# Kernel tuning notes

Measured on AMD Instinct MI355X. Metric: run time of the kernel, lower is better.

Reference implementation:

```python
import jax, jax.numpy as jnp
import numpy as np

BN_EPS = 1e-5

def _conv1x1(x, w, b):
    # x: (B,C,H,W), w: (O,C), b: (O,)
    return jnp.einsum('bchw,oc->bohw', x, w) + b[None, :, None, None]

def setup_inputs() -> dict:
    key = jax.random.key(0)
    ks = jax.random.split(key, 9)
    B, C, H, W = 16, 512, 64, 64
    Ci = C // 2
    x = jax.random.normal(ks[0], (B, C, H, W), dtype=jnp.float32)
    s_in = (2.0 / C) ** 0.5   # kaiming fan_out-ish scale for 1x1 conv
    s_ci = (2.0 / Ci) ** 0.5
    return {
        'x': x,
        'g_w': jax.random.normal(ks[1], (Ci, C), dtype=jnp.float32) * s_in,
        'g_b': jnp.zeros((Ci,), dtype=jnp.float32),
        'theta_w': jax.random.normal(ks[2], (Ci, C), dtype=jnp.float32) * s_in,
        'theta_b': jnp.zeros((Ci,), dtype=jnp.float32),
        'phi_w': jax.random.normal(ks[3], (Ci, C), dtype=jnp.float32) * s_in,
        'phi_b': jnp.zeros((Ci,), dtype=jnp.float32),
        'W_w': jax.random.normal(ks[4], (C, Ci), dtype=jnp.float32) * s_ci,
        'W_b': jnp.zeros((C,), dtype=jnp.float32),
        'bn_gamma': jnp.ones((C,), dtype=jnp.float32),
        'bn_beta': jnp.zeros((C,), dtype=jnp.float32),
    }

def reference(x, g_w, g_b, theta_w, theta_b, phi_w, phi_b, W_w, W_b, bn_gamma, bn_beta):
    B, C, H, W = x.shape
    N = H * W
    g_x = _conv1x1(x, g_w, g_b).reshape(B, -1, N)          # (B, Ci, N)
    theta_x = _conv1x1(x, theta_w, theta_b).reshape(B, -1, N)  # (B, Ci, N)
    phi_x = _conv1x1(x, phi_w, phi_b).reshape(B, -1, N)        # (B, Ci, N)
    # Faithful to source: theta NOT permuted -> f is (B, Ci, Ci) channel attention
    f = jnp.einsum('bcn,bdn->bcd', theta_x, phi_x)
    f_div_C = jax.nn.softmax(f, axis=-1)
    y = jnp.einsum('bcd,bdn->bcn', f_div_C, g_x).reshape(B, -1, H, W)  # (B, Ci, H, W)
    z = _conv1x1(y, W_w, W_b)                              # (B, C, H, W)
    # BatchNorm2d, training mode (batch statistics, biased var as in torch)
    mean = jnp.mean(z, axis=(0, 2, 3), keepdims=True)
    var = jnp.var(z, axis=(0, 2, 3), keepdims=True)
    z = (z - mean) * jax.lax.rsqrt(var + BN_EPS)
    z = z * bn_gamma[None, :, None, None] + bn_beta[None, :, None, None]
    return z + x
```

## Files before the change

### kernel.cpp

```cpp
#include <hip/hip_runtime.h>

typedef __bf16 bf16x8 __attribute__((ext_vector_type(8)));
typedef float f32x4 __attribute__((ext_vector_type(4)));

#define LDK 40
#define NB 16
#define C_ 512
#define CI 256
#define HW 4096

__device__ __forceinline__ float bf2f(unsigned short u){
  union { unsigned int u; float f; } c; c.u = ((unsigned int)u) << 16; return c.f;
}
__device__ __forceinline__ unsigned short f2bf(float f){
  union { float f; unsigned int u; } c; c.f = f;
  unsigned int u = c.u + 0x7fffu + ((c.u >> 16) & 1u);
  return (unsigned short)(u >> 16);
}
__device__ __forceinline__ float read_val(const void* p, int i, bool f32){
  return f32 ? ((const float*)p)[i] : bf2f(((const unsigned short*)p)[i]);
}


__device__ __forceinline__ void stage_rm(const unsigned short* __restrict__ src, int stride,
                                         unsigned short* dst, int t){
  #pragma unroll
  for (int it = 0; it < 2; ++it){
    int idx = t + it*256;
    int row = idx >> 2;
    int ko  = (idx & 3) * 8;
    *(uint4*)(dst + row*LDK + ko) = *(const uint4*)(src + (size_t)row*stride + ko);
  }
}

__device__ __forceinline__ void stage_rm_f32(const float* __restrict__ src, int stride,
                                             unsigned short* dh, unsigned short* dl, int t){
  #pragma unroll
  for (int it = 0; it < 4; ++it){
    int idx = t + it*256;
    int row = idx >> 3;
    int ko  = (idx & 7) * 4;
    f32x4 v = *(const f32x4*)(src + (size_t)row*stride + ko);
    #pragma unroll
    for (int e = 0; e < 4; ++e){
      float fv = v[e];
      unsigned short h = f2bf(fv);
      dh[row*LDK + ko + e] = h;
      dl[row*LDK + ko + e] = f2bf(fv - bf2f(h));
    }
  }
}

__device__ __forceinline__ void stage_tr(const unsigned short* __restrict__ src, int stride,
                                         unsigned short* dst, int t){
  #pragma unroll
  for (int it = 0; it < 2; ++it){
    int idx = t + it*256;
    int row = idx >> 4;
    int co  = (idx & 15) * 8;
    uint4 vv = *(const uint4*)(src + (size_t)row*stride + co);
    unsigned short e[8]; *(uint4*)e = vv;
    #pragma unroll
    for (int k = 0; k < 8; ++k) dst[(co + k)*LDK + row] = e[k];
  }
}

__device__ __forceinline__ void stage_tr_f32(const float* __restrict__ src, int stride,
                                             unsigned short* dst, int t){
  #pragma unroll
  for (int it = 0; it < 2; ++it){
    int idx = t + it*256;
    int row = idx >> 4;
    int co  = (idx & 15) * 8;
    f32x4 v0 = *(const f32x4*)(src + (size_t)row*stride + co);
    f32x4 v1 = *(const f32x4*)(src + (size_t)row*stride + co + 4);
    #pragma unroll
    for (int k = 0; k < 4; ++k){
      dst[(co + k)*LDK + row]     = f2bf(v0[k]);
      dst[(co + 4 + k)*LDK + row] = f2bf(v1[k]);
    }
  }
}

__device__ __forceinline__ void stage_split(const float* __restrict__ src, int stride,
                                            unsigned short* dh, unsigned short* dl, int t){
  stage_rm_f32(src, stride, dh, dl, t);
}

__device__ __forceinline__ void mfma_step(const unsigned short* As, const unsigned short* Bs,
                                          f32x4 acc[4][4], int wm, int wn, int lane){
  const int r = lane & 15, q = lane >> 4;
  bf16x8 a[4], b[4];
  #pragma unroll
  for (int i = 0; i < 4; ++i)
    a[i] = *(const bf16x8*)(As + (wm*64 + 16*i + r)*LDK + 8*q);
  #pragma unroll
  for (int j = 0; j < 4; ++j)
    b[j] = *(const bf16x8*)(Bs + (wn*64 + 16*j + r)*LDK + 8*q);
  #pragma unroll
  for (int i = 0; i < 4; ++i)
    #pragma unroll
    for (int j = 0; j < 4; ++j)
      acc[i][j] = __builtin_amdgcn_mfma_f32_16x16x32_bf16(a[i], b[j], acc[i][j], 0, 0, 0);
}

__global__ __launch_bounds__(256) void k_detect(const unsigned short* __restrict__ x, int* flag){
  const int t = threadIdx.x;
  int cnt = 0;
  for (int i = t; i < 65536; i += 256){
    unsigned short u = x[i];
    if (((u >> 7) & 0xFF) == 0xFF) cnt++;
  }
  __shared__ int red[256];
  red[t] = cnt; __syncthreads();
  for (int s2 = 128; s2 > 0; s2 >>= 1){
    if (t < s2) red[t] += red[t + s2];
    __syncthreads();
  }
  if (t == 0) flag[0] = (red[0] > 0) ? 1 : 0;
}

__global__ __launch_bounds__(256) void k_wconv(const void* tw, const void* pw, const void* gw,
    const void* Ww, const void* gb, const void* tb, const void* pb, const void* Wb,
    const void* gam, const void* bet, const int* __restrict__ flag,
    unsigned short* twh, unsigned short* twl, unsigned short* phh, unsigned short* phl,
    unsigned short* gwc, unsigned short* Wwc, float* biasf){
  const bool f32 = (*flag != 0);
  const int bid = blockIdx.x, t = threadIdx.x;
  if (bid < 2048){
    const int seg = bid >> 9;
    const int i = (bid & 511)*256 + t;
    if (seg == 0){
      float w = read_val(tw, i, f32);
      unsigned short h = f2bf(w);
      twh[i] = h; twl[i] = f2bf(w - bf2f(h));
    } else if (seg == 1){
      float w = read_val(pw, i, f32);
      unsigned short h = f2bf(w);
      phh[i] = h; phl[i] = f2bf(w - bf2f(h));
    } else if (seg == 2){
      gwc[i] = f2bf(read_val(gw, i, f32));
    } else {
      Wwc[i] = f2bf(read_val(Ww, i, f32));
    }
  } else {
    const int i = (bid - 2048)*256 + t;
    if (i < 2304){
      float v;
      if      (i <  256) v = read_val(gb,  i,        f32);
      else if (i <  512) v = read_val(tb,  i - 256,  f32);
      else if (i <  768) v = read_val(pb,  i - 512,  f32);
      else if (i < 1280) v = read_val(Wb,  i - 768,  f32);
      else if (i < 1792) v = read_val(gam, i - 1280, f32);
      else               v = read_val(bet, i - 1792, f32);
      biasf[i] = v;
    }
  }
}

__global__ __launch_bounds__(256) void k_gram(const void* __restrict__ xraw,
                                              const int* __restrict__ flag,
                                              float* __restrict__ G, float* __restrict__ s){
  const bool f32 = (*flag != 0);
  const int b = blockIdx.z, bn = blockIdx.x, bm = blockIdx.y;
  const int t = threadIdx.x, lane = t & 63, w = t >> 6, wm = w >> 1, wn = w & 1;
  __shared__ unsigned short Ah[128*LDK];
  __shared__ unsigned short Al[128*LDK];
  __shared__ unsigned short Bh[128*LDK];
  __shared__ unsigned short Bl[128*LDK];
  __shared__ float red[256];
  f32x4 acc[4][4] = {};
  float sacc = 0.f;
  const bool diag = (bm == bn);
  for (int k0 = 0; k0 < HW; k0 += 32){
    if (f32){
      const float* xb = (const float*)xraw + (size_t)b*C_*HW;
      stage_rm_f32(xb + (size_t)bm*128*HW + k0, HW, Ah, Al, t);
      if (!diag) stage_rm_f32(xb + (size_t)bn*128*HW + k0, HW, Bh, Bl, t);
    } else {
      const unsigned short* xb = (const unsigned short*)xraw + (size_t)b*C_*HW;
      stage_rm(xb + (size_t)bm*128*HW + k0, HW, Ah, t);
      if (!diag) stage_rm(xb + (size_t)bn*128*HW + k0, HW, Bh, t);
    }
    __syncthreads();
    const unsigned short* BhU = diag ? Ah : Bh;
    const unsigned short* BlU = diag ? Al : Bl;
    mfma_step(Ah, BhU, acc, wm, wn, lane);
    if (f32){
      mfma_step(Ah, BlU, acc, wm, wn, lane);
      mfma_step(Al, BhU, acc, wm, wn, lane);
    }
    if (diag){
      const int row = t >> 1, half = t & 1;
      const unsigned short* ph = Ah + row*LDK + half*16;
      const unsigned short* pl = Al + row*LDK + half*16;
      if (f32){
        #pragma unroll
        for (int e = 0; e < 16; ++e) sacc += bf2f(ph[e]) + bf2f(pl[e]);
      } else {
        #pragma unroll
        for (int e = 0; e < 16; ++e) sacc += bf2f(ph[e]);
      }
    }
    __syncthreads();
  }
  float* Gb = G + (size_t)b*C_*C_;
  const int r = lane & 15, q = lane >> 4;
  #pragma unroll
  for (int i = 0; i < 4; ++i)
    #pragma unroll
    for (int j = 0; j < 4; ++j)
      #pragma unroll
      for (int ii = 0; ii < 4; ++ii){
        int row = bm*128 + wm*64 + 16*i + 4*q + ii;
        int col = bn*128 + wn*64 + 16*j + r;
        Gb[(size_t)row*C_ + col] = acc[i][j][ii];
      }
  if (diag){
    red[t] = sacc;
    __syncthreads();
    if (t < 128) s[(size_t)b*C_ + bm*128 + t] = red[2*t] + red[2*t+1];
  }
}

__global__ __launch_bounds__(256) void k_gconv(const void* __restrict__ xraw,
    const int* __restrict__ flag, const unsigned short* __restrict__ gwc,
    const float* __restrict__ gbf, unsigned short* __restrict__ gT){
  const bool f32 = (*flag != 0);
  const int b = blockIdx.z, mt = blockIdx.x, nt = blockIdx.y;
  const int t = threadIdx.x, lane = t & 63, w = t >> 6, wm = w >> 1, wn = w & 1;
  __shared__ unsigned short As[128*LDK];
  __shared__ unsigned short Bs[128*LDK];
  f32x4 acc[4][4] = {};
  for (int k0 = 0; k0 < C_; k0 += 32){
    if (f32){
      const float* xb = (const float*)xraw + (size_t)b*C_*HW;
      stage_tr_f32(xb + (size_t)k0*HW + mt*128, HW, As, t);
    } else {
      const unsigned short* xb = (const unsigned short*)xraw + (size_t)b*C_*HW;
      stage_tr(xb + (size_t)k0*HW + mt*128, HW, As, t);
    }
    stage_rm(gwc + (size_t)nt*128*C_ + k0, C_, Bs, t);
    __syncthreads();
    mfma_step(As, Bs, acc, wm, wn, lane);
    __syncthreads();
  }
  unsigned short* gTb = gT + (size_t)b*HW*CI;
  const int r = lane & 15, q = lane >> 4;
  #pragma unroll
  for (int j = 0; j < 4; ++j){
    int col = nt*128 + wn*64 + 16*j + r;
    float bias = gbf[col];
    #pragma unroll
    for (int i = 0; i < 4; ++i)
      #pragma unroll
      for (int ii = 0; ii < 4; ++ii){
        int row = mt*128 + wm*64 + 16*i + 4*q + ii;
        gTb[(size_t)row*CI + col] = f2bf(acc[i][j][ii] + bias);
      }
  }
}

__global__ __launch_bounds__(256) void k_T(const unsigned short* __restrict__ twh,
    const unsigned short* __restrict__ twl, const int* __restrict__ flag,
    const float* __restrict__ G, unsigned short* __restrict__ Th, unsigned short* __restrict__ Tl){
  const bool f32 = (*flag != 0);
  const int b = blockIdx.z, nt = blockIdx.x, mt = blockIdx.y;
  const int t = threadIdx.x, lane = t & 63, w = t >> 6, wm = w >> 1, wn = w & 1;
  __shared__ unsigned short Ath[128*LDK];
  __shared__ unsigned short Atl[128*LDK];
  __shared__ unsigned short Bh[128*LDK];
  __shared__ unsigned short Bl[128*LDK];
  const float* Gb = G + (size_t)b*C_*C_;
  f32x4 acc[4][4] = {};
  for (int k0 = 0; k0 < C_; k0 += 32){
    stage_rm(twh + (size_t)mt*128*C_ + k0, C_, Ath, t);
    if (f32) stage_rm(twl + (size_t)mt*128*C_ + k0, C_, Atl, t);
    stage_split(Gb + (size_t)nt*128*C_ + k0, C_, Bh, Bl, t);
    __syncthreads();
    mfma_step(Ath, Bh, acc, wm, wn, lane);
    mfma_step(Ath, Bl, acc, wm, wn, lane);
    if (f32) mfma_step(Atl, Bh, acc, wm, wn, lane);
    __syncthreads();
  }
  unsigned short* Thb = Th + (size_t)b*CI*C_;
  unsigned short* Tlb = Tl + (size_t)b*CI*C_;
  const int r = lane & 15, q = lane >> 4;
  #pragma unroll
  for (int i = 0; i < 4; ++i)
    #pragma unroll
    for (int j = 0; j < 4; ++j)
      #pragma unroll
      for (int ii = 0; ii < 4; ++ii){
        int row = mt*128 + wm*64 + 16*i + 4*q + ii;
        int col = nt*128 + wn*64 + 16*j + r;
        float vv = acc[i][j][ii];
        unsigned short h = f2bf(vv);
        Thb[(size_t)row*C_ + col] = h;
        Tlb[(size_t)row*C_ + col] = f2bf(vv - bf2f(h));
      }
}

__global__ __launch_bounds__(256) void k_f(const unsigned short* __restrict__ Th,
    const unsigned short* __restrict__ Tl, const unsigned short* __restrict__ phh,
    const unsigned short* __restrict__ phl, const int* __restrict__ flag,
    float* __restrict__ f){
  const bool f32 = (*flag != 0);
  const int b = blockIdx.z, nt = blockIdx.x, mt = blockIdx.y;
  const int t = threadIdx.x, lane = t & 63, w = t >> 6, wm = w >> 1, wn = w & 1;
  __shared__ unsigned short ATh[128*LDK];
  __shared__ unsigned short ATl[128*LDK];
  __shared__ unsigned short Bph[128*LDK];
  __shared__ unsigned short Bpl[128*LDK];
  f32x4 acc[4][4] = {};
  const unsigned short* Thb = Th + (size_t)b*CI*C_;
  const unsigned short* Tlb = Tl + (size_t)b*CI*C_;
  for (int k0 = 0; k0 < C_; k0 += 32){
    stage_rm(Thb + (size_t)mt*128*C_ + k0, C_, ATh, t);
    stage_rm(Tlb + (size_t)mt*128*C_ + k0, C_, ATl, t);
    stage_rm(phh + (size_t)nt*128*C_ + k0, C_, Bph, t);
    if (f32) stage_rm(phl + (size_t)nt*128*C_ + k0, C_, Bpl, t);
    __syncthreads();
    mfma_step(ATh, Bph, acc, wm, wn, lane);
    mfma_step(ATl, Bph, acc, wm, wn, lane);
    if (f32) mfma_step(ATh, Bpl, acc, wm, wn, lane);
    __syncthreads();
  }
  float* fb = f + (size_t)b*CI*CI;
  const int r = lane & 15, q = lane >> 4;
  #pragma unroll
  for (int i = 0; i < 4; ++i)
    #pragma unroll
    for (int j = 0; j < 4; ++j)
      #pragma unroll
      for (int ii = 0; ii < 4; ++ii){
        int row = mt*128 + wm*64 + 16*i + 4*q + ii;
        int col = nt*128 + wn*64 + 16*j + r;
        fb[(size_t)row*CI + col] = acc[i][j][ii];
      }
}

__global__ __launch_bounds__(256) void k_uv(const unsigned short* __restrict__ twh,
    const unsigned short* __restrict__ twl, const unsigned short* __restrict__ phh,
    const unsigned short* __restrict__ phl, const float* __restrict__ s,
    float* __restrict__ u, float* __restrict__ v){
  const int b = blockIdx.x, c = threadIdx.x;
  __shared__ float sl[C_];
  sl[c] = s[(size_t)b*C_ + c];
  sl[c + 256] = s[(size_t)b*C_ + c + 256];
  __syncthreads();
  float su = 0.f, sv = 0.f;
  for (int e = 0; e < C_; ++e){
    su += (bf2f(twh[(size_t)c*C_ + e]) + bf2f(twl[(size_t)c*C_ + e])) * sl[e];
    sv += (bf2f(phh[(size_t)c*C_ + e]) + bf2f(phl[(size_t)c*C_ + e])) * sl[e];
  }
  u[(size_t)b*CI + c] = su;
  v[(size_t)b*CI + c] = sv;
}

__global__ __launch_bounds__(256) void k_softmax(const float* __restrict__ f,
    const float* __restrict__ u, const float* __restrict__ v,
    const float* __restrict__ tbf, const float* __restrict__ pbf,
    unsigned short* __restrict__ S){
  const int b = blockIdx.y;
  const int c = blockIdx.x*4 + (threadIdx.x >> 6);
  const int lane = threadIdx.x & 63;
  const float* fr = f + ((size_t)b*CI + c)*CI;
  f32x4 val = *(const f32x4*)(fr + lane*4);
  const float uc = u[(size_t)b*CI + c];
  const float tbc = tbf[c];
  float vv[4];
  #pragma unroll
  for (int k = 0; k < 4; ++k){
    int d = lane*4 + k;
    float pbd = pbf[d];
    vv[k] = val[k] + uc*pbd + tbc*(v[(size_t)b*CI + d] + 4096.0f*pbd);
  }
  float mx = fmaxf(fmaxf(vv[0], vv[1]), fmaxf(vv[2], vv[3]));
  #pragma unroll
  for (int off = 1; off < 64; off <<= 1) mx = fmaxf(mx, __shfl_xor(mx, off));
  float e[4], sum = 0.f;
  #pragma unroll
  for (int k = 0; k < 4; ++k){ e[k] = expf(vv[k] - mx); sum += e[k]; }
  #pragma unroll
  for (int off = 1; off < 64; off <<= 1) sum += __shfl_xor(sum, off);
  float inv = 1.0f / sum;
  uint2 pack;
  pack.x = (unsigned int)f2bf(e[0]*inv) | ((unsigned int)f2bf(e[1]*inv) << 16);
  pack.y = (unsigned int)f2bf(e[2]*inv) | ((unsigned int)f2bf(e[3]*inv) << 16);
  *(uint2*)(S + ((size_t)b*CI + c)*CI + lane*4) = pack;
}

__global__ __launch_bounds__(256) void k_M2(const unsigned short* __restrict__ Wwc,
                                            const unsigned short* __restrict__ S,
                                            unsigned short* __restrict__ M2){
  const int b = blockIdx.z, nt = blockIdx.x, mt = blockIdx.y;
  const int t = threadIdx.x, lane = t & 63, w = t >> 6, wm = w >> 1, wn = w & 1;
  __shared__ unsigned short As[128*LDK];
  __shared__ unsigned short Bs[128*LDK];
  f32x4 acc[4][4] = {};
  for (int k0 = 0; k0 < CI; k0 += 32){
    stage_rm(Wwc + (size_t)mt*128*CI + k0, CI, As, t);
    stage_tr(S + (size_t)b*CI*CI + (size_t)k0*CI + nt*128, CI, Bs, t);
    __syncthreads();
    mfma_step(As, Bs, acc, wm, wn, lane);
    __syncthreads();
  }
  unsigned short* M2b = M2 + (size_t)b*C_*CI;
  const int r = lane & 15, q = lane >> 4;
  #pragma unroll
  for (int i = 0; i < 4; ++i)
    #pragma unroll
    for (int j = 0; j < 4; ++j)
      #pragma unroll
      for (int ii = 0; ii < 4; ++ii){
        int row = mt*128 + wm*64 + 16*i + 4*q + ii;
        int col = nt*128 + wn*64 + 16*j + r;
        M2b[(size_t)row*CI + col] = f2bf(acc[i][j][ii]);
      }
}

__global__ __launch_bounds__(256) void k_z(const unsigned short* __restrict__ M2,
                                           const unsigned short* __restrict__ gT,
                                           const float* __restrict__ Wbf,
                                           unsigned short* __restrict__ z){
  const int b = blockIdx.z, nt = blockIdx.x, mt = blockIdx.y;
  const int t = threadIdx.x, lane = t & 63, w = t >> 6, wm = w >> 1, wn = w & 1;
  __shared__ unsigned short As[128*LDK];
  __shared__ unsigned short Bs[128*LDK];
  const unsigned short* M2b = M2 + (size_t)b*C_*CI;
  const unsigned short* gTb = gT + (size_t)b*HW*CI;
  f32x4 acc[4][4] = {};
  for (int k0 = 0; k0 < CI; k0 += 32){
    stage_rm(M2b + (size_t)mt*128*CI + k0, CI, As, t);
    stage_rm(gTb + (size_t)nt*128*CI + k0, CI, Bs, t);
    __syncthreads();
    mfma_step(As, Bs, acc, wm, wn, lane);
    __syncthreads();
  }
  unsigned short* zb = z + (size_t)b*C_*HW;
  const int r = lane & 15, q = lane >> 4;
  #pragma unroll
  for (int i = 0; i < 4; ++i)
    #pragma unroll
    for (int ii = 0; ii < 4; ++ii){
      int row = mt*128 + wm*64 + 16*i + 4*q + ii;
      float bias = Wbf[row];
      #pragma unroll
      for (int j = 0; j < 4; ++j){
        int col = nt*128 + wn*64 + 16*j + r;
        zb[(size_t)row*HW + col] = f2bf(acc[i][j][ii] + bias);
      }
    }
}

__global__ __launch_bounds__(256) void k_bnstats(const unsigned short* __restrict__ z,
    const float* __restrict__ gamf, const float* __restrict__ betf,
    float* __restrict__ scale, float* __restrict__ shift){
  const int o = blockIdx.x, t = threadIdx.x, lane = t & 63, w = t >> 6;
  float sum = 0.f, ss = 0.f;
  for (int b = 0; b < NB; ++b){
    const unsigned short* p = z + ((size_t)b*C_ + o)*HW + t*16;
    #pragma unroll
    for (int it = 0; it < 2; ++it){
      uint4 raw = *(const uint4*)(p + it*8);
      unsigned int wd[4] = {raw.x, raw.y, raw.z, raw.w};
      #pragma unroll
      for (int k = 0; k < 4; ++k){
        float f0 = bf2f((unsigned short)(wd[k] & 0xffff));
        float f1 = bf2f((unsigned short)(wd[k] >> 16));
        sum += f0 + f1; ss += f0*f0 + f1*f1;
      }
    }
  }
  #pragma unroll
  for (int off = 1; off < 64; off <<= 1){
    sum += __shfl_xor(sum, off);
    ss  += __shfl_xor(ss, off);
  }
  __shared__ float r1[4], r2[4];
  if (lane == 0){ r1[w] = sum; r2[w] = ss; }
  __syncthreads();
  if (t == 0){
    float S1 = r1[0]+r1[1]+r1[2]+r1[3];
    float S2 = r2[0]+r2[1]+r2[2]+r2[3];
    const float n = (float)NB * (float)HW;
    float mean = S1 / n;
    float var  = S2 / n - mean*mean;
    float sc = gamf[o] * rsqrtf(var + 1e-5f);
    scale[o] = sc;
    shift[o] = betf[o] - mean*sc;
  }
}

__global__ __launch_bounds__(256) void k_out(const unsigned short* __restrict__ z,
    const void* __restrict__ xraw, const int* __restrict__ flag,
    const float* __restrict__ scale, const float* __restrict__ shift, void* __restrict__ outraw){
  const bool f32 = (*flag != 0);
  const size_t g = (size_t)blockIdx.x*256 + threadIdx.x;
  const size_t base = g*8;
  const int o = (int)((base >> 12) & (C_ - 1));
  const float sc = scale[o], sh = shift[o];
  uint4 zr = *(const uint4*)(z + base);
  unsigned int zz[4] = {zr.x, zr.y, zr.z, zr.w};
  float zv[8];
  #pragma unroll
  for (int k = 0; k < 4; ++k){
    zv[2*k]   = bf2f((unsigned short)(zz[k] & 0xffff));
    zv[2*k+1] = bf2f((unsigned short)(zz[k] >> 16));
  }
  if (f32){
    const float* x = (const float*)xraw;
    float* out = (float*)outraw;
    f32x4 x0 = *(const f32x4*)(x + base);
    f32x4 x1 = *(const f32x4*)(x + base + 4);
    f32x4 o0, o1;
    #pragma unroll
    for (int k = 0; k < 4; ++k){
      o0[k] = zv[k]*sc + sh + x0[k];
      o1[k] = zv[4+k]*sc + sh + x1[k];
    }
    *(f32x4*)(out + base) = o0;
    *(f32x4*)(out + base + 4) = o1;
  } else {
    const unsigned short* x = (const unsigned short*)xraw;
    unsigned short* out = (unsigned short*)outraw;
    uint4 xr = *(const uint4*)(x + base);
    unsigned int xx[4] = {xr.x, xr.y, xr.z, xr.w};
    unsigned int res[4];
    #pragma unroll
    for (int k = 0; k < 4; ++k){
      float x0 = bf2f((unsigned short)(xx[k] & 0xffff));
      float x1 = bf2f((unsigned short)(xx[k] >> 16));
      res[k] = (unsigned int)f2bf(zv[2*k]*sc + sh + x0)
             | ((unsigned int)f2bf(zv[2*k+1]*sc + sh + x1) << 16);
    }
    uint4 ov; ov.x = res[0]; ov.y = res[1]; ov.z = res[2]; ov.w = res[3];
    *(uint4*)(out + base) = ov;
  }
}

extern "C" void kernel_launch(void* const* d_in, const int* in_sizes, int n_in,
                              void* d_out, int out_size, void* d_ws, size_t ws_size,
                              hipStream_t stream){
  (void)in_sizes; (void)n_in; (void)out_size;
  const void* x   = d_in[0];
  const void* g_w = d_in[1];
  const void* g_b = d_in[2];
  const void* t_w = d_in[3];
  const void* t_b = d_in[4];
  const void* p_w = d_in[5];
  const void* p_b = d_in[6];
  const void* W_w = d_in[7];
  const void* W_b = d_in[8];
  const void* gam = d_in[9];
  const void* bet = d_in[10];
  char* ws = (char*)d_ws;

  constexpr size_t OFF_FLAG = 0;
  constexpr size_t OFF_TWH = OFF_FLAG + 16;
  constexpr size_t OFF_TWL = OFF_TWH + (size_t)CI*C_*2;
  constexpr size_t OFF_PHH = OFF_TWL + (size_t)CI*C_*2;
  constexpr size_t OFF_PHL = OFF_PHH + (size_t)CI*C_*2;
  constexpr size_t OFF_GWC = OFF_PHL + (size_t)CI*C_*2;
  constexpr size_t OFF_WWC = OFF_GWC + (size_t)CI*C_*2;
  constexpr size_t OFF_BIA = OFF_WWC + (size_t)C_*CI*2;
  constexpr size_t OFF_G  = OFF_BIA + 2304*4;
  constexpr size_t OFF_S  = OFF_G  + (size_t)NB*C_*C_*4;
  constexpr size_t OFF_U  = OFF_S  + (size_t)NB*C_*4;
  constexpr size_t OFF_V  = OFF_U  + (size_t)NB*CI*4;
  constexpr size_t OFF_GT = OFF_V  + (size_t)NB*CI*4;
  constexpr size_t OFF_TH = OFF_GT + (size_t)NB*HW*CI*2;
  constexpr size_t OFF_TL = OFF_TH + (size_t)NB*CI*C_*2;
  constexpr size_t OFF_F  = OFF_TL + (size_t)NB*CI*C_*2;
  constexpr size_t OFF_SM = OFF_F  + (size_t)NB*CI*CI*4;
  constexpr size_t OFF_M2 = OFF_SM + (size_t)NB*CI*CI*2;
  constexpr size_t OFF_Z  = OFF_M2 + (size_t)NB*C_*CI*2;
  constexpr size_t OFF_SC = OFF_Z  + (size_t)NB*C_*HW*2;
  constexpr size_t OFF_SH = OFF_SC + (size_t)C_*4;
  constexpr size_t TOTAL  = OFF_SH + (size_t)C_*4;
  if (ws_size < TOTAL) return;

  int* flag = (int*)(ws + OFF_FLAG);
  unsigned short* twh = (unsigned short*)(ws + OFF_TWH);
  unsigned short* twl = (unsigned short*)(ws + OFF_TWL);
  unsigned short* phh = (unsigned short*)(ws + OFF_PHH);
  unsigned short* phl = (unsigned short*)(ws + OFF_PHL);
  unsigned short* gwc = (unsigned short*)(ws + OFF_GWC);
  unsigned short* Wwc = (unsigned short*)(ws + OFF_WWC);
  float* biasf = (float*)(ws + OFF_BIA);
  float* G  = (float*)(ws + OFF_G);
  float* s  = (float*)(ws + OFF_S);
  float* u  = (float*)(ws + OFF_U);
  float* v  = (float*)(ws + OFF_V);
  unsigned short* gT = (unsigned short*)(ws + OFF_GT);
  unsigned short* Th = (unsigned short*)(ws + OFF_TH);
  unsigned short* Tl = (unsigned short*)(ws + OFF_TL);
  float* f  = (float*)(ws + OFF_F);
  unsigned short* Sm = (unsigned short*)(ws + OFF_SM);
  unsigned short* M2 = (unsigned short*)(ws + OFF_M2);
  unsigned short* z  = (unsigned short*)(ws + OFF_Z);
  float* scale = (float*)(ws + OFF_SC);
  float* shift = (float*)(ws + OFF_SH);

  float* gbf = biasf;
  float* tbf = biasf + 256;
  float* pbf = biasf + 512;
  float* Wbf = biasf + 768;
  float* gamf = biasf + 1280;
  float* betf = biasf + 1792;

  dim3 blk(256);
  k_detect <<<dim3(1),         blk, 0, stream>>>((const unsigned short*)x, flag);
  k_wconv  <<<dim3(2057),      blk, 0, stream>>>(t_w, p_w, g_w, W_w, g_b, t_b, p_b, W_b,
                                                 gam, bet, flag, twh, twl, phh, phl, gwc, Wwc, biasf);
  k_gram   <<<dim3(4, 4, NB),  blk, 0, stream>>>(x, flag, G, s);
  k_gconv  <<<dim3(32, 2, NB), blk, 0, stream>>>(x, flag, gwc, gbf, gT);
  k_T      <<<dim3(4, 2, NB),  blk, 0, stream>>>(twh, twl, flag, G, Th, Tl);
  k_uv     <<<dim3(NB),        blk, 0, stream>>>(twh, twl, phh, phl, s, u, v);
  k_f      <<<dim3(2, 2, NB),  blk, 0, stream>>>(Th, Tl, phh, phl, flag, f);
  k_softmax<<<dim3(64, NB),    blk, 0, stream>>>(f, u, v, tbf, pbf, Sm);
  k_M2     <<<dim3(2, 4, NB),  blk, 0, stream>>>(Wwc, Sm, M2);
  k_z      <<<dim3(32, 4, NB), blk, 0, stream>>>(M2, gT, Wbf, z);
  k_bnstats<<<dim3(C_),        blk, 0, stream>>>(z, gamf, betf, scale, shift);
  k_out    <<<dim3(16384),     blk, 0, stream>>>(z, x, flag, scale, shift, d_out);
}
```

Baseline: 818.3 us.

## Pre-split x to bf16 hi/lo, split-K symmetric Gram with reduction kernel

Adds a pass that converts fp32 x once into bf16 hi/lo planes and computes per-channel sums. The Gram kernel now computes only the 10 upper-triangle tiles with K split four ways into partials. A new reduction kernel sums the partials and mirrors them into bf16 hi/lo G, which k_T then loads directly. k_gconv also reads the pre-converted x. The goal is more blocks for the Gram GEMM (originally only 256 blocks), no repeated fp32-to-bf16 conversion, and no symmetric duplicate work, at the cost of extra memory traffic for xh/xl and the partial buffers, which are aliased onto existing workspace.

```diff
diff --git a/kernel.cpp b/kernel.cpp
--- a/kernel.cpp
+++ b/kernel.cpp
@@ -8,6 +8,8 @@
 #define C_ 512
 #define CI 256
 #define HW 4096
+#define KSPLIT 4
+#define KCHUNK (HW / KSPLIT)
 
 __device__ __forceinline__ float bf2f(unsigned short u){
   union { unsigned int u; float f; } c; c.u = ((unsigned int)u) << 16; return c.f;
@@ -30,24 +32,6 @@
     int row = idx >> 2;
     int ko  = (idx & 3) * 8;
     *(uint4*)(dst + row*LDK + ko) = *(const uint4*)(src + (size_t)row*stride + ko);
-  }
-}
-
-__device__ __forceinline__ void stage_rm_f32(const float* __restrict__ src, int stride,
-                                             unsigned short* dh, unsigned short* dl, int t){
-  #pragma unroll
-  for (int it = 0; it < 4; ++it){
-    int idx = t + it*256;
-    int row = idx >> 3;
-    int ko  = (idx & 7) * 4;
-    f32x4 v = *(const f32x4*)(src + (size_t)row*stride + ko);
-    #pragma unroll
-    for (int e = 0; e < 4; ++e){
-      float fv = v[e];
-      unsigned short h = f2bf(fv);
-      dh[row*LDK + ko + e] = h;
-      dl[row*LDK + ko + e] = f2bf(fv - bf2f(h));
-    }
   }
 }
 
@@ -63,28 +47,6 @@
     #pragma unroll
     for (int k = 0; k < 8; ++k) dst[(co + k)*LDK + row] = e[k];
   }
-}
-
-__device__ __forceinline__ void stage_tr_f32(const float* __restrict__ src, int stride,
-                                             unsigned short* dst, int t){
-  #pragma unroll
-  for (int it = 0; it < 2; ++it){
-    int idx = t + it*256;
-    int row = idx >> 4;
-    int co  = (idx & 15) * 8;
-    f32x4 v0 = *(const f32x4*)(src + (size_t)row*stride + co);
-    f32x4 v1 = *(const f32x4*)(src + (size_t)row*stride + co + 4);
-    #pragma unroll
-    for (int k = 0; k < 4; ++k){
-      dst[(co + k)*LDK + row]     = f2bf(v0[k]);
-      dst[(co + 4 + k)*LDK + row] = f2bf(v1[k]);
-    }
-  }
-}
-
-__device__ __forceinline__ void stage_split(const float* __restrict__ src, int stride,
-                                            unsigned short* dh, unsigned short* dl, int t){
-  stage_rm_f32(src, stride, dh, dl, t);
 }
 
 __device__ __forceinline__ void mfma_step(const unsigned short* As, const unsigned short* Bs,
@@ -158,29 +120,80 @@
   }
 }
 
+__global__ __launch_bounds__(256) void k_xconv(const void* __restrict__ xraw,
+    const int* __restrict__ flag, unsigned short* __restrict__ xh,
+    unsigned short* __restrict__ xl, float* __restrict__ s){
+  const bool f32 = (*flag != 0);
+  const int bc = blockIdx.x, t = threadIdx.x;
+  float sum = 0.f;
+  if (f32){
+    const float* xr = (const float*)xraw + (size_t)bc*HW;
+    unsigned short* oh = xh + (size_t)bc*HW;
+    unsigned short* ol = xl + (size_t)bc*HW;
+    #pragma unroll
+    for (int it = 0; it < 4; ++it){
+      const int off = it*1024 + t*4;
+      f32x4 v = *(const f32x4*)(xr + off);
+      unsigned int wh[2], wl[2];
+      #pragma unroll
+      for (int k = 0; k < 2; ++k){
+        unsigned short h0 = f2bf(v[2*k]),   h1 = f2bf(v[2*k+1]);
+        unsigned short l0 = f2bf(v[2*k]   - bf2f(h0));
+        unsigned short l1 = f2bf(v[2*k+1] - bf2f(h1));
+        wh[k] = (unsigned int)h0 | ((unsigned int)h1 << 16);
+        wl[k] = (unsigned int)l0 | ((unsigned int)l1 << 16);
+      }
+      sum += v[0] + v[1] + v[2] + v[3];
+      *(uint2*)(oh + off) = make_uint2(wh[0], wh[1]);
+      *(uint2*)(ol + off) = make_uint2(wl[0], wl[1]);
+    }
+  } else {
+    const unsigned short* xr = (const unsigned short*)xraw + (size_t)bc*HW;
+    #pragma unroll
+    for (int it = 0; it < 2; ++it){
+      const int off = it*2048 + t*8;
+      uint4 raw = *(const uint4*)(xr + off);
+      unsigned int wd[4] = {raw.x, raw.y, raw.z, raw.w};
+      #pragma unroll
+      for (int k = 0; k < 4; ++k)
+        sum += bf2f((unsigned short)(wd[k] & 0xffff)) + bf2f((unsigned short)(wd[k] >> 16));
+    }
+  }
+  #pragma unroll
+  for (int off = 1; off < 64; off <<= 1) sum += __shfl_xor(sum, off);
+  __shared__ float r1[4];
+  if ((t & 63) == 0) r1[t >> 6] = sum;
+  __syncthreads();
+  if (t == 0) s[bc] = r1[0] + r1[1] + r1[2] + r1[3];
+}
+
 __global__ __launch_bounds__(256) void k_gram(const void* __restrict__ xraw,
-                                              const int* __restrict__ flag,
-                                              float* __restrict__ G, float* __restrict__ s){
+    const unsigned short* __restrict__ xh, const unsigned short* __restrict__ xl,
+    const int* __restrict__ flag, float* __restrict__ Gp){
   const bool f32 = (*flag != 0);
-  const int b = blockIdx.z, bn = blockIdx.x, bm = blockIdx.y;
+  const int b = blockIdx.z, ks = blockIdx.y, tile = blockIdx.x;
+  int bm, bn;
+  if      (tile < 4){ bm = 0; bn = tile; }
+  else if (tile < 7){ bm = 1; bn = tile - 3; }
+  else if (tile < 9){ bm = 2; bn = tile - 5; }
+  else              { bm = 3; bn = 3; }
   const int t = threadIdx.x, lane = t & 63, w = t >> 6, wm = w >> 1, wn = w & 1;
   __shared__ unsigned short Ah[128*LDK];
   __shared__ unsigned short Al[128*LDK];
   __shared__ unsigned short Bh[128*LDK];
   __shared__ unsigned short Bl[128*LDK];
-  __shared__ float red[256];
   f32x4 acc[4][4] = {};
-  float sacc = 0.f;
   const bool diag = (bm == bn);
-  for (int k0 = 0; k0 < HW; k0 += 32){
-    if (f32){
-      const float* xb = (const float*)xraw + (size_t)b*C_*HW;
-      stage_rm_f32(xb + (size_t)bm*128*HW + k0, HW, Ah, Al, t);
-      if (!diag) stage_rm_f32(xb + (size_t)bn*128*HW + k0, HW, Bh, Bl, t);
-    } else {
-      const unsigned short* xb = (const unsigned short*)xraw + (size_t)b*C_*HW;
-      stage_rm(xb + (size_t)bm*128*HW + k0, HW, Ah, t);
-      if (!diag) stage_rm(xb + (size_t)bn*128*HW + k0, HW, Bh, t);
+  const unsigned short* xhb = f32 ? (xh + (size_t)b*C_*HW)
+                                  : ((const unsigned short*)xraw + (size_t)b*C_*HW);
+  const unsigned short* xlb = xl + (size_t)b*C_*HW;
+  const int kbeg = ks*KCHUNK, kend = kbeg + KCHUNK;
+  for (int k0 = kbeg; k0 < kend; k0 += 32){
+    stage_rm(xhb + (size_t)(bm*128)*HW + k0, HW, Ah, t);
+    if (f32) stage_rm(xlb + (size_t)(bm*128)*HW + k0, HW, Al, t);
+    if (!diag){
+      stage_rm(xhb + (size_t)(bn*128)*HW + k0, HW, Bh, t);
+      if (f32) stage_rm(xlb + (size_t)(bn*128)*HW + k0, HW, Bl, t);
     }
     __syncthreads();
     const unsigned short* BhU = diag ? Ah : Bh;
@@ -190,41 +203,98 @@
       mfma_step(Ah, BlU, acc, wm, wn, lane);
       mfma_step(Al, BhU, acc, wm, wn, lane);
     }
-    if (diag){
-      const int row = t >> 1, half = t & 1;
-      const unsigned short* ph = Ah + row*LDK + half*16;
-      const unsigned short* pl = Al + row*LDK + half*16;
-      if (f32){
+    __syncthreads();
+  }
+  float* Gt = Gp + (((size_t)b*10 + tile)*KSPLIT + ks)*16384;
+  const int r = lane & 15, q = lane >> 4;
+  #pragma unroll
+  for (int i = 0; i < 4; ++i)
+    #pragma unroll
+    for (int j = 0; j < 4; ++j)
+      #pragma unroll
+      for (int ii = 0; ii < 4; ++ii){
+        int row = wm*64 + 16*i + 4*q + ii;
+        int col = wn*64 + 16*j + r;
+        Gt[row*128 + col] = acc[i][j][ii];
+      }
+}
+
+__global__ __launch_bounds__(256) void k_gred(const float* __restrict__ Gp,
+    unsigned short* __restrict__ Gh, unsigned short* __restrict__ Gl){
+  const int b = blockIdx.z, bmO = blockIdx.y, bnO = blockIdx.x, t = threadIdx.x;
+  const int lo = bmO < bnO ? bmO : bnO;
+  const int hi = bmO < bnO ? bnO : bmO;
+  const int tile = (lo == 0) ? hi : (lo == 1) ? 3 + hi : (lo == 2) ? 5 + hi : 9;
+  const float* src = Gp + ((size_t)b*10 + tile)*KSPLIT*16384;
+  unsigned short* ghB = Gh + (size_t)b*C_*C_;
+  unsigned short* glB = Gl + (size_t)b*C_*C_;
+  if (bmO <= bnO){
+    #pragma unroll
+    for (int i = 0; i < 16; ++i){
+      const int off = i*1024 + t*4;
+      f32x4 v = *(const f32x4*)(src + off);
+      #pragma unroll
+      for (int ks = 1; ks < KSPLIT; ++ks){
+        f32x4 u2 = *(const f32x4*)(src + ks*16384 + off);
+        v[0] += u2[0]; v[1] += u2[1]; v[2] += u2[2]; v[3] += u2[3];
+      }
+      const int row = off >> 7, col = off & 127;
+      unsigned int wh[2], wl[2];
+      #pragma unroll
+      for (int k = 0; k < 2; ++k){
+        unsigned short h0 = f2bf(v[2*k]),   h1 = f2bf(v[2*k+1]);
+        unsigned short l0 = f2bf(v[2*k]   - bf2f(h0));
+        unsigned short l1 = f2bf(v[2*k+1] - bf2f(h1));
+        wh[k] = (unsigned int)h0 | ((unsigned int)h1 << 16);
+        wl[k] = (unsigned int)l0 | ((unsigned int)l1 << 16);
+      }
+      size_t o = (size_t)(bmO*128 + row)*C_ + bnO*128 + col;
+      *(uint2*)(ghB + o) = make_uint2(wh[0], wh[1]);
+      *(uint2*)(glB + o) = make_uint2(wl[0], wl[1]);
+    }
+  } else {
+    __shared__ float ldz[32*129];
+    const int rr = t >> 1, cseg = (t & 1)*16;
+    const int orl = t >> 3, oseg = (t & 7)*16;
+    for (int cc = 0; cc < 4; ++cc){
+      float vals[16];
+      #pragma unroll
+      for (int j = 0; j < 4; ++j){
+        const int so = rr*128 + cc*32 + cseg + j*4;
+        f32x4 v = *(const f32x4*)(src + so);
         #pragma unroll
-        for (int e = 0; e < 16; ++e) sacc += bf2f(ph[e]) + bf2f(pl[e]);
-      } else {
-        #pragma unroll
-        for (int e = 0; e < 16; ++e) sacc += bf2f(ph[e]);
-      }
-    }
-    __syncthreads();
-  }
-  float* Gb = G + (size_t)b*C_*C_;
-  const int r = lane & 15, q = lane >> 4;
-  #pragma unroll
-  for (int i = 0; i < 4; ++i)
-    #pragma unroll
-    for (int j = 0; j < 4; ++j)
-      #pragma unroll
-      for (int ii = 0; ii < 4; ++ii){
-        int row = bm*128 + wm*64 + 16*i + 4*q + ii;
-        int col = bn*128 + wn*64 + 16*j + r;
-        Gb[(size_t)row*C_ + col] = acc[i][j][ii];
-      }
-  if (diag){
-    red[t] = sacc;
-    __syncthreads();
-    if (t < 128) s[(size_t)b*C_ + bm*128 + t] = red[2*t] + red[2*t+1];
+        for (int ks = 1; ks < KSPLIT; ++ks){
+          f32x4 u2 = *(const f32x4*)(src + ks*16384 + so);
+          v[0] += u2[0]; v[1] += u2[1]; v[2] += u2[2]; v[3] += u2[3];
+        }
+        vals[4*j] = v[0]; vals[4*j+1] = v[1]; vals[4*j+2] = v[2]; vals[4*j+3] = v[3];
+      }
+      __syncthreads();
+      #pragma unroll
+      for (int e = 0; e < 16; ++e) ldz[(cseg + e)*129 + rr] = vals[e];
+      __syncthreads();
+      unsigned int wh[8], wl[8];
+      #pragma unroll
+      for (int k = 0; k < 8; ++k){
+        float f0 = ldz[orl*129 + oseg + 2*k];
+        float f1 = ldz[orl*129 + oseg + 2*k + 1];
+        unsigned short h0 = f2bf(f0), h1 = f2bf(f1);
+        unsigned short l0 = f2bf(f0 - bf2f(h0)), l1 = f2bf(f1 - bf2f(h1));
+        wh[k] = (unsigned int)h0 | ((unsigned int)h1 << 16);
+        wl[k] = (unsigned int)l0 | ((unsigned int)l1 << 16);
+      }
+      size_t o = (size_t)(bmO*128 + cc*32 + orl)*C_ + bnO*128 + oseg;
+      *(uint4*)(ghB + o)     = make_uint4(wh[0], wh[1], wh[2], wh[3]);
+      *(uint4*)(ghB + o + 8) = make_uint4(wh[4], wh[5], wh[6], wh[7]);
+      *(uint4*)(glB + o)     = make_uint4(wl[0], wl[1], wl[2], wl[3]);
+      *(uint4*)(glB + o + 8) = make_uint4(wl[4], wl[5], wl[6], wl[7]);
+    }
   }
 }
 
 __global__ __launch_bounds__(256) void k_gconv(const void* __restrict__ xraw,
-    const int* __restrict__ flag, const unsigned short* __restrict__ gwc,
+    const int* __restrict__ flag, const unsigned short* __restrict__ xh,
+    const unsigned short* __restrict__ gwc,
     const float* __restrict__ gbf, unsigned short* __restrict__ gT){
   const bool f32 = (*flag != 0);
   const int b = blockIdx.z, mt = blockIdx.x, nt = blockIdx.y;
@@ -232,14 +302,10 @@
   __shared__ unsigned short As[128*LDK];
   __shared__ unsigned short Bs[128*LDK];
   f32x4 acc[4][4] = {};
+  const unsigned short* xb = f32 ? (xh + (size_t)b*C_*HW)
+                                 : ((const unsigned short*)xraw + (size_t)b*C_*HW);
   for (int k0 = 0; k0 < C_; k0 += 32){
-    if (f32){
-      const float* xb = (const float*)xraw + (size_t)b*C_*HW;
-      stage_tr_f32(xb + (size_t)k0*HW + mt*128, HW, As, t);
-    } else {
-      const unsigned short* xb = (const unsigned short*)xraw + (size_t)b*C_*HW;
-      stage_tr(xb + (size_t)k0*HW + mt*128, HW, As, t);
-    }
+    stage_tr(xb + (size_t)k0*HW + mt*128, HW, As, t);
     stage_rm(gwc + (size_t)nt*128*C_ + k0, C_, Bs, t);
     __syncthreads();
     mfma_step(As, Bs, acc, wm, wn, lane);
@@ -263,7 +329,8 @@
 
 __global__ __launch_bounds__(256) void k_T(const unsigned short* __restrict__ twh,
     const unsigned short* __restrict__ twl, const int* __restrict__ flag,
-    const float* __restrict__ G, unsigned short* __restrict__ Th, unsigned short* __restrict__ Tl){
+    const unsigned short* __restrict__ Gh, const unsigned short* __restrict__ Gl,
+    unsigned short* __restrict__ Th, unsigned short* __restrict__ Tl){
   const bool f32 = (*flag != 0);
   const int b = blockIdx.z, nt = blockIdx.x, mt = blockIdx.y;
   const int t = threadIdx.x, lane = t & 63, w = t >> 6, wm = w >> 1, wn = w & 1;
@@ -271,12 +338,14 @@
   __shared__ unsigned short Atl[128*LDK];
   __shared__ unsigned short Bh[128*LDK];
   __shared__ unsigned short Bl[128*LDK];
-  const float* Gb = G + (size_t)b*C_*C_;
+  const unsigned short* Ghb = Gh + (size_t)b*C_*C_;
+  const unsigned short* Glb = Gl + (size_t)b*C_*C_;
   f32x4 acc[4][4] = {};
   for (int k0 = 0; k0 < C_; k0 += 32){
     stage_rm(twh + (size_t)mt*128*C_ + k0, C_, Ath, t);
     if (f32) stage_rm(twl + (size_t)mt*128*C_ + k0, C_, Atl, t);
-    stage_split(Gb + (size_t)nt*128*C_ + k0, C_, Bh, Bl, t);
+    stage_rm(Ghb + (size_t)nt*128*C_ + k0, C_, Bh, t);
+    stage_rm(Glb + (size_t)nt*128*C_ + k0, C_, Bl, t);
     __syncthreads();
     mfma_step(Ath, Bh, acc, wm, wn, lane);
     mfma_step(Ath, Bl, acc, wm, wn, lane);
@@ -565,8 +634,9 @@
   constexpr size_t OFF_GWC = OFF_PHL + (size_t)CI*C_*2;
   constexpr size_t OFF_WWC = OFF_GWC + (size_t)CI*C_*2;
   constexpr size_t OFF_BIA = OFF_WWC + (size_t)C_*CI*2;
-  constexpr size_t OFF_G  = OFF_BIA + 2304*4;
-  constexpr size_t OFF_S  = OFF_G  + (size_t)NB*C_*C_*4;
+  constexpr size_t OFF_GH = OFF_BIA + 2304*4;
+  constexpr size_t OFF_GL = OFF_GH + (size_t)NB*C_*C_*2;
+  constexpr size_t OFF_S  = OFF_GL + (size_t)NB*C_*C_*2;
   constexpr size_t OFF_U  = OFF_S  + (size_t)NB*C_*4;
   constexpr size_t OFF_V  = OFF_U  + (size_t)NB*CI*4;
   constexpr size_t OFF_GT = OFF_V  + (size_t)NB*CI*4;
@@ -578,7 +648,10 @@
   constexpr size_t OFF_Z  = OFF_M2 + (size_t)NB*C_*CI*2;
   constexpr size_t OFF_SC = OFF_Z  + (size_t)NB*C_*HW*2;
   constexpr size_t OFF_SH = OFF_SC + (size_t)C_*4;
-  constexpr size_t TOTAL  = OFF_SH + (size_t)C_*4;
+  constexpr size_t OFF_XH = OFF_SH + (size_t)C_*4;
+  constexpr size_t TOTAL  = OFF_XH + (size_t)NB*C_*HW*2;
+  static_assert((size_t)NB*10*KSPLIT*16384*4 ==
+                (size_t)NB*HW*CI*2 + 2*(size_t)NB*CI*C_*2, "Gp alias size");
   if (ws_size < TOTAL) return;
 
   int* flag = (int*)(ws + OFF_FLAG);
@@ -589,7 +662,8 @@
   unsigned short* gwc = (unsigned short*)(ws + OFF_GWC);
   unsigned short* Wwc = (unsigned short*)(ws + OFF_WWC);
   float* biasf = (float*)(ws + OFF_BIA);
-  float* G  = (float*)(ws + OFF_G);
+  unsigned short* Gh = (unsigned short*)(ws + OFF_GH);
+  unsigned short* Gl = (unsigned short*)(ws + OFF_GL);
   float* s  = (float*)(ws + OFF_S);
   float* u  = (float*)(ws + OFF_U);
   float* v  = (float*)(ws + OFF_V);
@@ -602,6 +676,9 @@
   unsigned short* z  = (unsigned short*)(ws + OFF_Z);
   float* scale = (float*)(ws + OFF_SC);
   float* shift = (float*)(ws + OFF_SH);
+  unsigned short* xh = (unsigned short*)(ws + OFF_XH);
+  unsigned short* xl = (unsigned short*)(ws + OFF_Z);
+  float* Gp = (float*)(ws + OFF_GT);
 
   float* gbf = biasf;
   float* tbf = biasf + 256;
@@ -611,17 +688,19 @@
   float* betf = biasf + 1792;
 
   dim3 blk(256);
-  k_detect <<<dim3(1),         blk, 0, stream>>>((const unsigned short*)x, flag);
-  k_wconv  <<<dim3(2057),      blk, 0, stream>>>(t_w, p_w, g_w, W_w, g_b, t_b, p_b, W_b,
-                                                 gam, bet, flag, twh, twl, phh, phl, gwc, Wwc, biasf);
-  k_gram   <<<dim3(4, 4, NB),  blk, 0, stream>>>(x, flag, G, s);
-  k_gconv  <<<dim3(32, 2, NB), blk, 0, stream>>>(x, flag, gwc, gbf, gT);
-  k_T      <<<dim3(4, 2, NB),  blk, 0, stream>>>(twh, twl, flag, G, Th, Tl);
-  k_uv     <<<dim3(NB),        blk, 0, stream>>>(twh, twl, phh, phl, s, u, v);
-  k_f      <<<dim3(2, 2, NB),  blk, 0, stream>>>(Th, Tl, phh, phl, flag, f);
-  k_softmax<<<dim3(64, NB),    blk, 0, stream>>>(f, u, v, tbf, pbf, Sm);
-  k_M2     <<<dim3(2, 4, NB),  blk, 0, stream>>>(Wwc, Sm, M2);
-  k_z      <<<dim3(32, 4, NB), blk, 0, stream>>>(M2, gT, Wbf, z);
-  k_bnstats<<<dim3(C_),        blk, 0, stream>>>(z, gamf, betf, scale, shift);
-  k_out    <<<dim3(16384),     blk, 0, stream>>>(z, x, flag, scale, shift, d_out);
-}
+  k_detect <<<dim3(1),          blk, 0, stream>>>((const unsigned short*)x, flag);
+  k_wconv  <<<dim3(2057),       blk, 0, stream>>>(t_w, p_w, g_w, W_w, g_b, t_b, p_b, W_b,
+                                                  gam, bet, flag, twh, twl, phh, phl, gwc, Wwc, biasf);
+  k_xconv  <<<dim3(NB*C_),      blk, 0, stream>>>(x, flag, xh, xl, s);
+  k_gram   <<<dim3(10, KSPLIT, NB), blk, 0, stream>>>(x, xh, xl, flag, Gp);
+  k_gred   <<<dim3(4, 4, NB),   blk, 0, stream>>>(Gp, Gh, Gl);
+  k_gconv  <<<dim3(32, 2, NB),  blk, 0, stream>>>(x, flag, xh, gwc, gbf, gT);
+  k_T      <<<dim3(4, 2, NB),   blk, 0, stream>>>(twh, twl, flag, Gh, Gl, Th, Tl);
+  k_uv     <<<dim3(NB),         blk, 0, stream>>>(twh, twl, phh, phl, s, u, v);
+  k_f      <<<dim3(2, 2, NB),   blk, 0, stream>>>(Th, Tl, phh, phl, flag, f);
+  k_softmax<<<dim3(64, NB),     blk, 0, stream>>>(f, u, v, tbf, pbf, Sm);
+  k_M2     <<<dim3(2, 4, NB),   blk, 0, stream>>>(Wwc, Sm, M2);
+  k_z      <<<dim3(32, 4, NB),  blk, 0, stream>>>(M2, gT, Wbf, z);
+  k_bnstats<<<dim3(C_),         blk, 0, stream>>>(z, gamf, betf, scale, shift);
+  k_out    <<<dim3(16384),      blk, 0, stream>>>(z, x, flag, scale, shift, d_out);
+}
```

Measured after the change: 856.3 us. 4.6% more time.
